# Optimization experiments

Measured on AMD Instinct MI355X. Metric: run time of the kernel, lower is better.

Reference implementation:

```python
import jax, jax.numpy as jnp
import numpy as np

B, S, D, H = 64, 512, 256, 512  # batch, seq_len, input embed dim, LSTM hidden dim


def setup_inputs() -> dict:
    key = jax.random.key(0)
    k1, k2, k3, k4, k5 = jax.random.split(key, 5)
    scale = 1.0 / np.sqrt(H)
    return {
        "state_embeds": jax.random.normal(k1, (B, S, D), dtype=jnp.float32),
        "W_ih": jax.random.normal(k2, (4 * H, D), dtype=jnp.float32) * scale,
        "W_hh": jax.random.normal(k3, (4 * H, H), dtype=jnp.float32) * scale,
        "b_ih": jax.random.normal(k4, (4 * H,), dtype=jnp.float32) * scale,
        "b_hh": jax.random.normal(k5, (4 * H,), dtype=jnp.float32) * scale,
        "h0": jnp.zeros((B, H), dtype=jnp.float32),
        "c0": jnp.zeros((B, H), dtype=jnp.float32),
    }


def reference(state_embeds, W_ih, W_hh, b_ih, b_hh, h0, c0):
    # Precompute the input projection for all timesteps at once: [B, S, 4H]
    x_proj = jnp.einsum("bsd,gd->bsg", state_embeds, W_ih) + b_ih + b_hh

    def step(carry, xt):
        h, c = carry
        gates = xt + h @ W_hh.T  # [B, 4H]
        i, f, g, o = jnp.split(gates, 4, axis=-1)
        i = jax.nn.sigmoid(i)
        f = jax.nn.sigmoid(f)
        g = jnp.tanh(g)
        o = jax.nn.sigmoid(o)
        c_new = f * c + i * g
        h_new = o * jnp.tanh(c_new)
        return (h_new, c_new), h_new

    (hT, cT), hs = jax.lax.scan(step, (h0, c0), jnp.swapaxes(x_proj, 0, 1))
    embeddings = jnp.swapaxes(hs, 0, 1)  # [B, S, H]
    # hidden state is detached in the original; here we just return it
    return embeddings, hT, cT
```

## Files before the change

### kernel.cpp

```cpp
#include <hip/hip_runtime.h>
#include <hip/hip_bf16.h>


#define NB 64
#define NS 512
#define ND 256
#define NH 512
#define FLAG_MAGIC 0x41000000

typedef __bf16 bf16x8 __attribute__((ext_vector_type(8)));
typedef float  f32x4  __attribute__((ext_vector_type(4)));

union Frag {
  bf16x8 v;
  unsigned long long u[2];
  __bf16 e[8];
};

__device__ __forceinline__ float bf2f(__bf16 b) {
  unsigned short us = __builtin_bit_cast(unsigned short, b);
  unsigned int ui = ((unsigned int)us) << 16;
  return __builtin_bit_cast(float, ui);
}

__device__ __forceinline__ void hilo8(const float* vals, Frag& fh, Frag& fl) {
#pragma unroll
  for (int j = 0; j < 8; ++j) {
    __bf16 hi = (__bf16)vals[j];
    float r = vals[j] - bf2f(hi);
    fh.e[j] = hi;
    fl.e[j] = (__bf16)r;
  }
}

__device__ __forceinline__ float fsigmoid(float x) {
  return 1.0f / (1.0f + __expf(-x));
}
__device__ __forceinline__ float ftanh(float x) {
  float t = fminf(fmaxf(2.0f * x, -30.0f), 30.0f);
  float e = __expf(t);
  return (e - 1.0f) / (e + 1.0f);
}

__global__ __launch_bounds__(128, 1)
void lstm_persistent(const float* __restrict__ x,
                     const float* __restrict__ Wih,
                     const float* __restrict__ Whh,
                     const float* __restrict__ bih,
                     const float* __restrict__ bhh,
                     const float* __restrict__ h0,
                     const float* __restrict__ c0,
                     float* __restrict__ out,
                     int* __restrict__ flags,
                     unsigned short* __restrict__ hplane,
                     unsigned short* __restrict__ lplane)
{
  const int tid  = threadIdx.x;
  const int lane = tid & 63;
  const int wv   = tid >> 6;
  const int team = blockIdx.x >> 6;
  const int wg   = blockIdx.x & 63;
  const int l15  = lane & 15;
  const int quad = lane >> 4;
  const int hb   = wg * 8 + wv * 4;
  const int myb  = team * 16 + l15;
  const int myh  = hb + quad;

  int* flagsT = flags + team * 64;
  if (tid == 0)
    __hip_atomic_store(flagsT + wg, FLAG_MAGIC, __ATOMIC_RELAXED,
                       __HIP_MEMORY_SCOPE_AGENT);

  const int jA = l15 >> 2;
  const int gA = l15 & 3;
  const int rA = gA * NH + hb + jA;
  bf16x8 Ahi[24], Alo[24];
  {
    const float* wi = Wih + rA * ND;
    const float* wh = Whh + rA * NH;
#pragma unroll
    for (int c = 0; c < 24; ++c) {
      int k0 = c * 32 + quad * 8;
      const float* src = (c < 8) ? (wi + k0) : (wh + (k0 - 256));
      float4 f0 = *(const float4*)(src);
      float4 f1 = *(const float4*)(src + 4);
      float vals[8] = {f0.x, f0.y, f0.z, f0.w, f1.x, f1.y, f1.z, f1.w};
      Frag fh, fl;
      hilo8(vals, fh, fl);
      Ahi[c] = fh.v;
      Alo[c] = fl.v;
    }
  }

  float bias[4];
#pragma unroll
  for (int g = 0; g < 4; ++g)
    bias[g] = bih[g * NH + myh] + bhh[g * NH + myh];

  float c_st  = c0[myb * NH + myh];
  float h_val = 0.0f;

  const int planeHalf = NB * NH;

#pragma unroll 1
  for (int t = 0; t < NS; ++t) {
    float4 xf[16];
    const float* xr = x + (myb * NS + t) * ND + quad * 8;
#pragma unroll
    for (int c = 0; c < 8; ++c) {
      xf[2 * c]     = *(const float4*)(xr + 32 * c);
      xf[2 * c + 1] = *(const float4*)(xr + 32 * c + 4);
    }

    f32x4 a_hh = {bias[0], bias[1], bias[2], bias[3]};
    f32x4 a_hl = {0.f, 0.f, 0.f, 0.f};
    f32x4 a_lh = {0.f, 0.f, 0.f, 0.f};

#pragma unroll
    for (int c = 0; c < 8; ++c) {
      float vals[8] = {xf[2*c].x, xf[2*c].y, xf[2*c].z, xf[2*c].w,
                       xf[2*c+1].x, xf[2*c+1].y, xf[2*c+1].z, xf[2*c+1].w};
      Frag bh, bl;
      hilo8(vals, bh, bl);
      a_hh = __builtin_amdgcn_mfma_f32_16x16x32_bf16(Ahi[c], bh.v, a_hh, 0, 0, 0);
      a_hl = __builtin_amdgcn_mfma_f32_16x16x32_bf16(Ahi[c], bl.v, a_hl, 0, 0, 0);
      a_lh = __builtin_amdgcn_mfma_f32_16x16x32_bf16(Alo[c], bh.v, a_lh, 0, 0, 0);
    }

    if (t > 0) {
      while (true) {
        int fl = __hip_atomic_load(flagsT + lane, __ATOMIC_RELAXED,
                                   __HIP_MEMORY_SCOPE_AGENT);
        unsigned int d = (unsigned int)(fl - FLAG_MAGIC);
        if (__all(d >= (unsigned int)t && d <= 512u)) break;
        __builtin_amdgcn_s_sleep(1);
      }
      asm volatile("" ::: "memory");

      const int par = (t + 1) & 1;
      const unsigned short* hbp = hplane + par * planeHalf + myb * NH + quad * 8;
      const unsigned short* lbp = lplane + par * planeHalf + myb * NH + quad * 8;
#pragma unroll
      for (int c = 8; c < 24; ++c) {
        int off = 32 * (c - 8);
        Frag bh, bl;
        bh.u[0] = __hip_atomic_load((const unsigned long long*)(hbp + off),
                                    __ATOMIC_RELAXED, __HIP_MEMORY_SCOPE_AGENT);
        bh.u[1] = __hip_atomic_load((const unsigned long long*)(hbp + off + 4),
                                    __ATOMIC_RELAXED, __HIP_MEMORY_SCOPE_AGENT);
        bl.u[0] = __hip_atomic_load((const unsigned long long*)(lbp + off),
                                    __ATOMIC_RELAXED, __HIP_MEMORY_SCOPE_AGENT);
        bl.u[1] = __hip_atomic_load((const unsigned long long*)(lbp + off + 4),
                                    __ATOMIC_RELAXED, __HIP_MEMORY_SCOPE_AGENT);
        a_hh = __builtin_amdgcn_mfma_f32_16x16x32_bf16(Ahi[c], bh.v, a_hh, 0, 0, 0);
        a_hl = __builtin_amdgcn_mfma_f32_16x16x32_bf16(Ahi[c], bl.v, a_hl, 0, 0, 0);
        a_lh = __builtin_amdgcn_mfma_f32_16x16x32_bf16(Alo[c], bh.v, a_lh, 0, 0, 0);
      }
    } else {
      const float* hr = h0 + myb * NH + quad * 8;
#pragma unroll
      for (int c = 8; c < 24; ++c) {
        int off = 32 * (c - 8);
        float4 f0 = *(const float4*)(hr + off);
        float4 f1 = *(const float4*)(hr + off + 4);
        float vals[8] = {f0.x, f0.y, f0.z, f0.w, f1.x, f1.y, f1.z, f1.w};
        Frag bh, bl;
        hilo8(vals, bh, bl);
        a_hh = __builtin_amdgcn_mfma_f32_16x16x32_bf16(Ahi[c], bh.v, a_hh, 0, 0, 0);
        a_hl = __builtin_amdgcn_mfma_f32_16x16x32_bf16(Ahi[c], bl.v, a_hl, 0, 0, 0);
        a_lh = __builtin_amdgcn_mfma_f32_16x16x32_bf16(Alo[c], bh.v, a_lh, 0, 0, 0);
      }
    }

    float pre_i = a_hh[0] + a_hl[0] + a_lh[0];
    float pre_f = a_hh[1] + a_hl[1] + a_lh[1];
    float pre_g = a_hh[2] + a_hl[2] + a_lh[2];
    float pre_o = a_hh[3] + a_hl[3] + a_lh[3];
    float gi = fsigmoid(pre_i);
    float gf = fsigmoid(pre_f);
    float gg = ftanh(pre_g);
    float go = fsigmoid(pre_o);
    c_st  = gf * c_st + gi * gg;
    h_val = go * ftanh(c_st);

    out[(myb * NS + t) * NH + myh] = h_val;

    __bf16 hh = (__bf16)h_val;
    float  rr = h_val - bf2f(hh);
    __bf16 hl = (__bf16)rr;
    unsigned int uh = (unsigned int)__builtin_bit_cast(unsigned short, hh);
    unsigned int ul = (unsigned int)__builtin_bit_cast(unsigned short, hl);
    unsigned int ph = (unsigned int)__shfl_xor((int)uh, 16, 64);
    unsigned int pl = (unsigned int)__shfl_xor((int)ul, 16, 64);
    if ((quad & 1) == 0) {
      int par  = t & 1;
      int eoff = par * planeHalf + myb * NH + myh;
      __hip_atomic_store((unsigned int*)(hplane + eoff), uh | (ph << 16),
                         __ATOMIC_RELAXED, __HIP_MEMORY_SCOPE_AGENT);
      __hip_atomic_store((unsigned int*)(lplane + eoff), ul | (pl << 16),
                         __ATOMIC_RELAXED, __HIP_MEMORY_SCOPE_AGENT);
    }

    asm volatile("s_waitcnt vmcnt(0)" ::: "memory");
    __syncthreads();
    if (tid == 0)
      __hip_atomic_store(flagsT + wg, FLAG_MAGIC + t + 1, __ATOMIC_RELAXED,
                         __HIP_MEMORY_SCOPE_AGENT);
  }

  const int obase = NB * NS * NH;
  out[obase + myb * NH + myh] = h_val;
  out[obase + NB * NH + myb * NH + myh] = c_st;
}

extern "C" void kernel_launch(void* const* d_in, const int* in_sizes, int n_in,
                              void* d_out, int out_size, void* d_ws, size_t ws_size,
                              hipStream_t stream) {
  const float* x   = (const float*)d_in[0];
  const float* Wih = (const float*)d_in[1];
  const float* Whh = (const float*)d_in[2];
  const float* bih = (const float*)d_in[3];
  const float* bhh = (const float*)d_in[4];
  const float* h0  = (const float*)d_in[5];
  const float* c0  = (const float*)d_in[6];
  float* out = (float*)d_out;

  char* ws = (char*)d_ws;
  int* flags = (int*)ws;
  unsigned short* hplane = (unsigned short*)(ws + 1024);
  unsigned short* lplane = (unsigned short*)(ws + 1024 + 2 * NB * NH * 2);

  lstm_persistent<<<dim3(256), dim3(128), 0, stream>>>(
      x, Wih, Whh, bih, bhh, h0, c0, out, flags, hplane, lplane);
}
```

Measured before the change: 5.245 ms.

## Use per-timestep h ring buffer to avoid double-buffer reuse and atomic loads

Adds a ring-buffer variant that writes each timestep's bf16 hi/lo hidden state to its own slot instead of a two-slot ping-pong. Since slots are never overwritten, reads of the previous hidden state become plain 16-byte vector loads rather than pairs of 64-bit atomic loads. The output store is also moved after the flag release, taking it off the critical path. In exchange it needs about 64 MB of workspace and falls back to the old kernel when the workspace is smaller. Plain loads might also hit stale cache lines, since correctness relies on the relaxed flag plus compiler barrier.

```diff
diff --git a/kernel.cpp b/kernel.cpp
--- a/kernel.cpp
+++ b/kernel.cpp
@@ -7,6 +7,7 @@
 #define ND 256
 #define NH 512
 #define FLAG_MAGIC 0x41000000
+#define PLANE_ELEMS (NB * NH)
 
 typedef __bf16 bf16x8 __attribute__((ext_vector_type(8)));
 typedef float  f32x4  __attribute__((ext_vector_type(4)));
@@ -40,6 +41,167 @@
   float t = fminf(fmaxf(2.0f * x, -30.0f), 30.0f);
   float e = __expf(t);
   return (e - 1.0f) / (e + 1.0f);
+}
+
+__global__ __launch_bounds__(128, 1)
+void lstm_ring(const float* __restrict__ x,
+               const float* __restrict__ Wih,
+               const float* __restrict__ Whh,
+               const float* __restrict__ bih,
+               const float* __restrict__ bhh,
+               const float* __restrict__ h0,
+               const float* __restrict__ c0,
+               float* __restrict__ out,
+               int* __restrict__ flags,
+               unsigned short* __restrict__ hring,
+               unsigned short* __restrict__ lring)
+{
+  const int tid  = threadIdx.x;
+  const int lane = tid & 63;
+  const int wv   = tid >> 6;
+  const int team = blockIdx.x >> 6;
+  const int wg   = blockIdx.x & 63;
+  const int l15  = lane & 15;
+  const int quad = lane >> 4;
+  const int hb   = wg * 8 + wv * 4;
+  const int myb  = team * 16 + l15;
+  const int myh  = hb + quad;
+
+  int* flagsT = flags + team * 64;
+  if (tid == 0)
+    __hip_atomic_store(flagsT + wg, FLAG_MAGIC, __ATOMIC_RELAXED,
+                       __HIP_MEMORY_SCOPE_AGENT);
+
+  const int jA = l15 >> 2;
+  const int gA = l15 & 3;
+  const int rA = gA * NH + hb + jA;
+  bf16x8 Ahi[24], Alo[24];
+  {
+    const float* wi = Wih + rA * ND;
+    const float* wh = Whh + rA * NH;
+#pragma unroll
+    for (int c = 0; c < 24; ++c) {
+      int k0 = c * 32 + quad * 8;
+      const float* src = (c < 8) ? (wi + k0) : (wh + (k0 - 256));
+      float4 f0 = *(const float4*)(src);
+      float4 f1 = *(const float4*)(src + 4);
+      float vals[8] = {f0.x, f0.y, f0.z, f0.w, f1.x, f1.y, f1.z, f1.w};
+      Frag fh, fl;
+      hilo8(vals, fh, fl);
+      Ahi[c] = fh.v;
+      Alo[c] = fl.v;
+    }
+  }
+
+  float bias[4];
+#pragma unroll
+  for (int g = 0; g < 4; ++g)
+    bias[g] = bih[g * NH + myh] + bhh[g * NH + myh];
+
+  float c_st  = c0[myb * NH + myh];
+  float h_val = 0.0f;
+
+#pragma unroll 1
+  for (int t = 0; t < NS; ++t) {
+    float4 xf[16];
+    const float* xr = x + (myb * NS + t) * ND + quad * 8;
+#pragma unroll
+    for (int c = 0; c < 8; ++c) {
+      xf[2 * c]     = *(const float4*)(xr + 32 * c);
+      xf[2 * c + 1] = *(const float4*)(xr + 32 * c + 4);
+    }
+
+    f32x4 a_hh = {bias[0], bias[1], bias[2], bias[3]};
+    f32x4 a_hl = {0.f, 0.f, 0.f, 0.f};
+    f32x4 a_lh = {0.f, 0.f, 0.f, 0.f};
+
+#pragma unroll
+    for (int c = 0; c < 8; ++c) {
+      float vals[8] = {xf[2*c].x, xf[2*c].y, xf[2*c].z, xf[2*c].w,
+                       xf[2*c+1].x, xf[2*c+1].y, xf[2*c+1].z, xf[2*c+1].w};
+      Frag bh, bl;
+      hilo8(vals, bh, bl);
+      a_hh = __builtin_amdgcn_mfma_f32_16x16x32_bf16(Ahi[c], bh.v, a_hh, 0, 0, 0);
+      a_hl = __builtin_amdgcn_mfma_f32_16x16x32_bf16(Ahi[c], bl.v, a_hl, 0, 0, 0);
+      a_lh = __builtin_amdgcn_mfma_f32_16x16x32_bf16(Alo[c], bh.v, a_lh, 0, 0, 0);
+    }
+
+    if (t > 0) {
+      while (true) {
+        int fl = __hip_atomic_load(flagsT + lane, __ATOMIC_RELAXED,
+                                   __HIP_MEMORY_SCOPE_AGENT);
+        unsigned int d = (unsigned int)(fl - FLAG_MAGIC);
+        if (__all(d >= (unsigned int)t && d <= 512u)) break;
+        __builtin_amdgcn_s_sleep(1);
+      }
+      asm volatile("" ::: "memory");
+
+      const unsigned short* hbp = hring + (t - 1) * PLANE_ELEMS + myb * NH + quad * 8;
+      const unsigned short* lbp = lring + (t - 1) * PLANE_ELEMS + myb * NH + quad * 8;
+#pragma unroll
+      for (int c = 8; c < 24; ++c) {
+        int off = 32 * (c - 8);
+        Frag bh, bl;
+        bh.v = *(const bf16x8*)(hbp + off);
+        bl.v = *(const bf16x8*)(lbp + off);
+        a_hh = __builtin_amdgcn_mfma_f32_16x16x32_bf16(Ahi[c], bh.v, a_hh, 0, 0, 0);
+        a_hl = __builtin_amdgcn_mfma_f32_16x16x32_bf16(Ahi[c], bl.v, a_hl, 0, 0, 0);
+        a_lh = __builtin_amdgcn_mfma_f32_16x16x32_bf16(Alo[c], bh.v, a_lh, 0, 0, 0);
+      }
+    } else {
+      const float* hr = h0 + myb * NH + quad * 8;
+#pragma unroll
+      for (int c = 8; c < 24; ++c) {
+        int off = 32 * (c - 8);
+        float4 f0 = *(const float4*)(hr + off);
+        float4 f1 = *(const float4*)(hr + off + 4);
+        float vals[8] = {f0.x, f0.y, f0.z, f0.w, f1.x, f1.y, f1.z, f1.w};
+        Frag bh, bl;
+        hilo8(vals, bh, bl);
+        a_hh = __builtin_amdgcn_mfma_f32_16x16x32_bf16(Ahi[c], bh.v, a_hh, 0, 0, 0);
+        a_hl = __builtin_amdgcn_mfma_f32_16x16x32_bf16(Ahi[c], bl.v, a_hl, 0, 0, 0);
+        a_lh = __builtin_amdgcn_mfma_f32_16x16x32_bf16(Alo[c], bh.v, a_lh, 0, 0, 0);
+      }
+    }
+
+    float pre_i = a_hh[0] + a_hl[0] + a_lh[0];
+    float pre_f = a_hh[1] + a_hl[1] + a_lh[1];
+    float pre_g = a_hh[2] + a_hl[2] + a_lh[2];
+    float pre_o = a_hh[3] + a_hl[3] + a_lh[3];
+    float gi = fsigmoid(pre_i);
+    float gf = fsigmoid(pre_f);
+    float gg = ftanh(pre_g);
+    float go = fsigmoid(pre_o);
+    c_st  = gf * c_st + gi * gg;
+    h_val = go * ftanh(c_st);
+
+    __bf16 hh = (__bf16)h_val;
+    float  rr = h_val - bf2f(hh);
+    __bf16 hl = (__bf16)rr;
+    unsigned int uh = (unsigned int)__builtin_bit_cast(unsigned short, hh);
+    unsigned int ul = (unsigned int)__builtin_bit_cast(unsigned short, hl);
+    unsigned int ph = (unsigned int)__shfl_xor((int)uh, 16, 64);
+    unsigned int pl = (unsigned int)__shfl_xor((int)ul, 16, 64);
+    if ((quad & 1) == 0) {
+      int eoff = t * PLANE_ELEMS + myb * NH + myh;
+      __hip_atomic_store((unsigned int*)(hring + eoff), uh | (ph << 16),
+                         __ATOMIC_RELAXED, __HIP_MEMORY_SCOPE_AGENT);
+      __hip_atomic_store((unsigned int*)(lring + eoff), ul | (pl << 16),
+                         __ATOMIC_RELAXED, __HIP_MEMORY_SCOPE_AGENT);
+    }
+
+    asm volatile("s_waitcnt vmcnt(0)" ::: "memory");
+    __syncthreads();
+    if (tid == 0)
+      __hip_atomic_store(flagsT + wg, FLAG_MAGIC + t + 1, __ATOMIC_RELAXED,
+                         __HIP_MEMORY_SCOPE_AGENT);
+
+    out[(myb * NS + t) * NH + myh] = h_val;
+  }
+
+  const int obase = NB * NS * NH;
+  out[obase + myb * NH + myh] = h_val;
+  out[obase + NB * NH + myb * NH + myh] = c_st;
 }
 
 __global__ __launch_bounds__(128, 1)
@@ -99,7 +261,6 @@
 
   float c_st  = c0[myb * NH + myh];
   float h_val = 0.0f;
-
   const int planeHalf = NB * NH;
 
 #pragma unroll 1
@@ -227,9 +388,19 @@
 
   char* ws = (char*)d_ws;
   int* flags = (int*)ws;
-  unsigned short* hplane = (unsigned short*)(ws + 1024);
-  unsigned short* lplane = (unsigned short*)(ws + 1024 + 2 * NB * NH * 2);
-
-  lstm_persistent<<<dim3(256), dim3(128), 0, stream>>>(
-      x, Wih, Whh, bih, bhh, h0, c0, out, flags, hplane, lplane);
-}
+
+  const size_t ringBytes = (size_t)NS * PLANE_ELEMS * sizeof(unsigned short);
+  const size_t need = 4096 + 2 * ringBytes;
+
+  if (ws_size >= need) {
+    unsigned short* hring = (unsigned short*)(ws + 4096);
+    unsigned short* lring = (unsigned short*)(ws + 4096 + ringBytes);
+    lstm_ring<<<dim3(256), dim3(128), 0, stream>>>(
+        x, Wih, Whh, bih, bhh, h0, c0, out, flags, hring, lring);
+  } else {
+    unsigned short* hplane = (unsigned short*)(ws + 4096);
+    unsigned short* lplane = (unsigned short*)(ws + 4096 + 2 * NB * NH * 2);
+    lstm_persistent<<<dim3(256), dim3(128), 0, stream>>>(
+        x, Wih, Whh, bih, bhh, h0, c0, out, flags, hplane, lplane);
+  }
+}
```

Result: faster. 4.604 ms (-12.2%).
